# Optimization experiments

Measured on AMD Instinct MI355X. Metric: run time of the kernel, lower is better.

## Reference

```python
import jax, jax.numpy as jnp
import numpy as np

KERNEL_SIZE = 21
SIGMA = 3.0


def _gaussian_kernel_2d(kernel_size, sigma, dtype):
    ax = jnp.arange(kernel_size, dtype=dtype) - (kernel_size - 1) / 2.0
    xx, yy = jnp.meshgrid(ax, ax, indexing='ij')
    k = jnp.exp(-(xx ** 2 + yy ** 2) / (2.0 * sigma ** 2))
    return k / jnp.sum(k)


def setup_inputs() -> dict:
    key = jax.random.key(0)
    x = jax.random.normal(key, (32, 3, 512, 512), dtype=jnp.float32)
    return {"x": x}


def reference(x):
    B, C, H, W = x.shape
    k2d = _gaussian_kernel_2d(KERNEL_SIZE, SIGMA, x.dtype)  # [K, K]
    # depthwise weights: OIHW with feature_group_count=C -> [C, 1, K, K]
    w = jnp.broadcast_to(k2d[None, None], (C, 1, KERNEL_SIZE, KERNEL_SIZE))
    pad = KERNEL_SIZE // 2
    x_pad = jnp.pad(x, ((0, 0), (0, 0), (pad, pad), (pad, pad)), mode='reflect')
    y = jax.lax.conv_general_dilated(
        x_pad, w,
        window_strides=(1, 1),
        padding='VALID',
        dimension_numbers=('NCHW', 'OIHW', 'NCHW'),
        feature_group_count=C,
    )
    return y
```

## Files before the change

kernel.cpp:

```cpp
#include <hip/hip_runtime.h>

#define HH  512
#define WW  512
#define RAD 10
#define KK  21
#define SEG 16
#define NROWS (SEG + 2 * RAD)
#define LSTRIDE 540

__global__ __launch_bounds__(256, 4) void gauss_blur_kernel(
    const float* __restrict__ x, float* __restrict__ out)
{
    const float wt[KK] = {
        0.00051432f, 0.00147793f, 0.00380033f, 0.00874446f, 0.01800488f,
        0.03317359f, 0.05469399f, 0.08069227f, 0.10652936f, 0.12584957f,
        0.13303907f,
        0.12584957f, 0.10652936f, 0.08069227f, 0.05469399f, 0.03317359f,
        0.01800488f, 0.00874446f, 0.00380033f, 0.00147793f, 0.00051432f
    };

    __shared__ __align__(16) float vbuf[SEG * LSTRIDE];

    const int t   = threadIdx.x;
    const int c0  = 2 * t;
    const int c1  = c0 + 1;
    const int y0  = blockIdx.x * SEG;
    const int img = blockIdx.y;

    const float* xim = x   + (size_t)img * (HH * WW);
    float*       oim = out + (size_t)img * (HH * WW);

    float2 rows[NROWS];
    #pragma unroll
    for (int i = 0; i < NROWS; ++i) {
        int r  = y0 - RAD + i;
        int rr = r < 0 ? -r : (r > HH - 1 ? 2 * (HH - 1) - r : r);
        rows[i] = *(const float2*)(xim + rr * WW + c0);
    }

    #pragma unroll
    for (int r = 0; r < SEG; ++r) {
        float vx = 0.f, vy = 0.f;
        #pragma unroll
        for (int k = 0; k < KK; ++k) {
            vx = fmaf(wt[k], rows[r + k].x, vx);
            vy = fmaf(wt[k], rows[r + k].y, vy);
        }
        float* vb = vbuf + r * LSTRIDE;
        *(float2*)(vb + RAD + c0) = make_float2(vx, vy);
        if (c0 >= 1 && c0 <= RAD)           vb[RAD - c0] = vx;
        if (c1 <= RAD)                      vb[RAD - c1] = vy;
        if (c0 >= WW - 11 && c0 <= WW - 2)  vb[RAD + 2 * (WW - 1) - c0] = vx;
        if (c1 >= WW - 11 && c1 <= WW - 2)  vb[RAD + 2 * (WW - 1) - c1] = vy;
    }

    __syncthreads();

    #pragma unroll
    for (int task = 0; task < 2; ++task) {
        const int tid = t + task * 256;
        const int r   = tid & (SEG - 1);
        const int q   = tid >> 4;
        const float* vr = vbuf + r * LSTRIDE + q * 16;

        float wnd[36];
        #pragma unroll
        for (int j = 0; j < 9; ++j) {
            float4 v4 = *(const float4*)(vr + 4 * j);
            wnd[4*j]   = v4.x; wnd[4*j+1] = v4.y;
            wnd[4*j+2] = v4.z; wnd[4*j+3] = v4.w;
        }

        float acc[16];
        #pragma unroll
        for (int j = 0; j < 16; ++j) {
            float s = 0.f;
            #pragma unroll
            for (int k = 0; k < KK; ++k)
                s = fmaf(wt[k], wnd[j + k], s);
            acc[j] = s;
        }

        float* op = oim + (size_t)(y0 + r) * WW + q * 16;
        #pragma unroll
        for (int j = 0; j < 4; ++j)
            *(float4*)(op + 4 * j) =
                make_float4(acc[4*j], acc[4*j+1], acc[4*j+2], acc[4*j+3]);
    }
}

extern "C" void kernel_launch(void* const* d_in, const int* in_sizes, int n_in,
                              void* d_out, int out_size, void* d_ws, size_t ws_size,
                              hipStream_t stream) {
    const float* x = (const float*)d_in[0];
    float* out = (float*)d_out;
    const int n_img = in_sizes[0] / (HH * WW);
    dim3 grid(HH / SEG, n_img);
    gauss_blur_kernel<<<grid, dim3(256), 0, stream>>>(x, out);
}
```

Before: 188.0 us.

## Use 512-thread blocks with one column per thread and XCD-aware block remap

Doubles the block to 512 threads so each thread handles one column in the vertical pass and one 16-wide task in the horizontal pass, halving per-thread register arrays. It also remaps block IDs so consecutive tiles of the same image land on the same XCD (assuming 8 XCDs), which should improve L2 reuse of the overlapping halo rows. The remap assumes the grid size divides by 8, and the vertical loads become 4-byte rather than 8-byte accesses.

```diff
diff --git a/kernel.cpp b/kernel.cpp
--- a/kernel.cpp
+++ b/kernel.cpp
@@ -8,7 +8,7 @@
 #define NROWS (SEG + 2 * RAD)
 #define LSTRIDE 540
 
-__global__ __launch_bounds__(256, 4) void gauss_blur_kernel(
+__global__ __launch_bounds__(512, 8) void gauss_blur_kernel(
     const float* __restrict__ x, float* __restrict__ out)
 {
     const float wt[KK] = {
@@ -21,72 +21,66 @@
 
     __shared__ __align__(16) float vbuf[SEG * LSTRIDE];
 
-    const int t   = threadIdx.x;
-    const int c0  = 2 * t;
-    const int c1  = c0 + 1;
-    const int y0  = blockIdx.x * SEG;
-    const int img = blockIdx.y;
+    const int bid = blockIdx.y * gridDim.x + blockIdx.x;
+    const int cpx = (gridDim.x * gridDim.y) >> 3;
+    const int lid = (bid & 7) * cpx + (bid >> 3);
+    const int y0  = (lid & 31) * SEG;
+    const int img = lid >> 5;
+
+    const int t = threadIdx.x;
 
     const float* xim = x   + (size_t)img * (HH * WW);
     float*       oim = out + (size_t)img * (HH * WW);
 
-    float2 rows[NROWS];
+    float rows[NROWS];
     #pragma unroll
     for (int i = 0; i < NROWS; ++i) {
         int r  = y0 - RAD + i;
         int rr = r < 0 ? -r : (r > HH - 1 ? 2 * (HH - 1) - r : r);
-        rows[i] = *(const float2*)(xim + rr * WW + c0);
+        rows[i] = xim[rr * WW + t];
     }
 
     #pragma unroll
     for (int r = 0; r < SEG; ++r) {
-        float vx = 0.f, vy = 0.f;
+        float v = 0.f;
         #pragma unroll
-        for (int k = 0; k < KK; ++k) {
-            vx = fmaf(wt[k], rows[r + k].x, vx);
-            vy = fmaf(wt[k], rows[r + k].y, vy);
-        }
+        for (int k = 0; k < KK; ++k)
+            v = fmaf(wt[k], rows[r + k], v);
         float* vb = vbuf + r * LSTRIDE;
-        *(float2*)(vb + RAD + c0) = make_float2(vx, vy);
-        if (c0 >= 1 && c0 <= RAD)           vb[RAD - c0] = vx;
-        if (c1 <= RAD)                      vb[RAD - c1] = vy;
-        if (c0 >= WW - 11 && c0 <= WW - 2)  vb[RAD + 2 * (WW - 1) - c0] = vx;
-        if (c1 >= WW - 11 && c1 <= WW - 2)  vb[RAD + 2 * (WW - 1) - c1] = vy;
+        vb[RAD + t] = v;
+        if (t >= 1 && t <= RAD)                   vb[RAD - t] = v;
+        if (t >= WW - 1 - RAD && t <= WW - 2)     vb[RAD + 2 * (WW - 1) - t] = v;
     }
 
     __syncthreads();
 
+    const int r = t & (SEG - 1);
+    const int q = t >> 4;
+    const float* vr = vbuf + r * LSTRIDE + q * 16;
+
+    float wnd[36];
     #pragma unroll
-    for (int task = 0; task < 2; ++task) {
-        const int tid = t + task * 256;
-        const int r   = tid & (SEG - 1);
-        const int q   = tid >> 4;
-        const float* vr = vbuf + r * LSTRIDE + q * 16;
+    for (int j = 0; j < 9; ++j) {
+        float4 v4 = *(const float4*)(vr + 4 * j);
+        wnd[4*j]   = v4.x; wnd[4*j+1] = v4.y;
+        wnd[4*j+2] = v4.z; wnd[4*j+3] = v4.w;
+    }
 
-        float wnd[36];
+    float acc[16];
+    #pragma unroll
+    for (int j = 0; j < 16; ++j) {
+        float s = 0.f;
         #pragma unroll
-        for (int j = 0; j < 9; ++j) {
-            float4 v4 = *(const float4*)(vr + 4 * j);
-            wnd[4*j]   = v4.x; wnd[4*j+1] = v4.y;
-            wnd[4*j+2] = v4.z; wnd[4*j+3] = v4.w;
-        }
+        for (int k = 0; k < KK; ++k)
+            s = fmaf(wt[k], wnd[j + k], s);
+        acc[j] = s;
+    }
 
-        float acc[16];
-        #pragma unroll
-        for (int j = 0; j < 16; ++j) {
-            float s = 0.f;
-            #pragma unroll
-            for (int k = 0; k < KK; ++k)
-                s = fmaf(wt[k], wnd[j + k], s);
-            acc[j] = s;
-        }
-
-        float* op = oim + (size_t)(y0 + r) * WW + q * 16;
-        #pragma unroll
-        for (int j = 0; j < 4; ++j)
-            *(float4*)(op + 4 * j) =
-                make_float4(acc[4*j], acc[4*j+1], acc[4*j+2], acc[4*j+3]);
-    }
+    float* op = oim + (size_t)(y0 + r) * WW + q * 16;
+    #pragma unroll
+    for (int j = 0; j < 4; ++j)
+        *(float4*)(op + 4 * j) =
+            make_float4(acc[4*j], acc[4*j+1], acc[4*j+2], acc[4*j+3]);
 }
 
 extern "C" void kernel_launch(void* const* d_in, const int* in_sizes, int n_in,
@@ -96,5 +90,5 @@
     float* out = (float*)d_out;
     const int n_img = in_sizes[0] / (HH * WW);
     dim3 grid(HH / SEG, n_img);
-    gauss_blur_kernel<<<grid, dim3(256), 0, stream>>>(x, out);
+    gauss_blur_kernel<<<grid, dim3(512), 0, stream>>>(x, out);
 }
```

New measurement: 183.0 us. 2.7% less time.
